# Optimization experiments

Measured on AMD Instinct MI355X. Metric: run time of the kernel, lower is better.

## Reference

```python
import jax, jax.numpy as jnp
import numpy as np

B, N, E, P = 8, 4096, 16384, 64   # batch, num_nodes, num_edges, query poses per scene
D, H, MSG, UPD = 256, 512, 256, 254  # node_dim, MLP hidden, msg_sz, update_sz


def setup_inputs() -> dict:
    key = jax.random.key(0)
    ks = jax.random.split(key, 12)
    s = 0.02  # weight scale
    inp = {
        'nodes_states': jax.random.normal(ks[0], (B, N, D), jnp.float32),
        'attn': jax.random.uniform(ks[1], (B, P, N), jnp.float32),
        'W_e1': (jax.random.normal(ks[2], (2 * D, H), jnp.float32) * s),
        'b_e1': jnp.zeros((H,), jnp.float32),
        'W_e2': (jax.random.normal(ks[3], (H, MSG), jnp.float32) * s),
        'b_e2': jnp.zeros((MSG,), jnp.float32),
        'W_n1': (jax.random.normal(ks[4], (D + MSG, H), jnp.float32) * s),
        'b_n1': jnp.zeros((H,), jnp.float32),
        'W_n2': (jax.random.normal(ks[5], (H, UPD), jnp.float32) * s),
        'b_n2': jnp.zeros((UPD,), jnp.float32),
        'edge_sources': jax.random.randint(ks[6], (E,), 0, N, jnp.int32),
        'edge_sinks': jax.random.randint(ks[7], (E,), 0, N, jnp.int32),
        'msg_steps': 3,
    }
    return inp


def reference(nodes_states, attn, W_e1, b_e1, W_e2, b_e2, W_n1, b_n1, W_n2, b_n2,
              edge_sources, edge_sinks, msg_steps):
    ns = nodes_states  # (B, N, D)
    upd_sz = W_n2.shape[-1]
    for _ in range(int(msg_steps)):
        # gather node states along edges
        src = ns[:, edge_sources]            # (B, E, D)
        snk = ns[:, edge_sinks]              # (B, E, D)
        e_in = jnp.concatenate([src, snk], axis=-1)          # (B, E, 2D)
        h = jax.nn.relu(e_in @ W_e1 + b_e1)
        msgs = h @ W_e2 + b_e2                               # (B, E, MSG)
        # scatter-add messages to sink nodes (== torch index_add on dim 1)
        incoming = jnp.zeros((ns.shape[0], ns.shape[1], msgs.shape[-1]), ns.dtype)
        incoming = incoming.at[:, edge_sinks].add(msgs)      # (B, N, MSG)
        # node update MLP
        n_in = jnp.concatenate([incoming, ns], axis=-1)      # (B, N, D+MSG)
        h2 = jax.nn.relu(n_in @ W_n1 + b_n1)
        upd = h2 @ W_n2 + b_n2                               # (B, N, UPD)
        ns = ns.at[:, :, -upd_sz:].add(upd)
    # graph_out_to_out: attention-weighted extraction (torch.bmm)
    extraction = jnp.einsum('bpn,bnd->bpd', attn, ns)        # (B, P, D)
    # num_copies = 0 -> extraction unchanged; unsqueeze(-1).unsqueeze(-1)
    return extraction[..., None, None]
```

## Files before the change

kernel.cpp:

```cpp
#include <hip/hip_runtime.h>
#include <cstddef>
#include <cstdint>

typedef unsigned short u16;
typedef unsigned int u32;
typedef short bf16x8 __attribute__((ext_vector_type(8)));
typedef float f32x4 __attribute__((ext_vector_type(4)));
typedef u32 u32x4 __attribute__((ext_vector_type(4)));

namespace {
constexpr int B_ = 8, N_ = 4096, E_ = 16384, P_ = 64;
constexpr int D_ = 256, H_ = 512, MSG_ = 256, UPD_ = 254;
constexpr int CHUNK_U16 = 16384;
constexpr int NCHUNK = 24;
constexpr float FXS = 16384.0f;
constexpr float FXI = 1.0f / 16384.0f;
}

__device__ inline u16 f2b(float f) {
  u32 u = __float_as_uint(f);
  u += 0x7FFFu + ((u >> 16) & 1u);
  return (u16)(u >> 16);
}
__device__ inline u32 pk2(float a, float b) {
  return (u32)f2b(a) | ((u32)f2b(b) << 16);
}
__device__ inline f32x4 mfma16(bf16x8 a, bf16x8 b, f32x4 c) {
  return __builtin_amdgcn_mfma_f32_16x16x32_bf16(a, b, c, 0, 0, 0);
}
__device__ inline void gload16(const void* g, void* l) {
  __builtin_amdgcn_global_load_lds(
      (const __attribute__((address_space(1))) unsigned int*)g,
      (__attribute__((address_space(3))) unsigned int*)l, 16, 0, 0);
}
__device__ inline void wait_vm0()   { asm volatile("s_waitcnt vmcnt(0)" ::: "memory"); }
__device__ inline void wait_lgkm0() { asm volatile("s_waitcnt lgkmcnt(0)" ::: "memory"); }
__device__ inline void chunk_boundary() {
  wait_lgkm0();
  wait_vm0();
  __builtin_amdgcn_s_barrier();
  __builtin_amdgcn_sched_barrier(0);
}

__device__ inline int wperm(int s) {
  return (s < 16) ? ((s >> 2) * 8 + (s & 3)) : (((s - 16) >> 2) * 8 + 4 + (s & 3));
}

__global__ void hist_k(const int* __restrict__ esnk, int* __restrict__ cnt) {
  const int e = blockIdx.x * 256 + threadIdx.x;
  atomicAdd(&cnt[esnk[e]], 1);
}
__global__ __launch_bounds__(256)
void scan_k(const int* __restrict__ cnt, int* __restrict__ rowptr,
            int* __restrict__ cursor) {
  __shared__ int part[257];
  const int t = threadIdx.x;
  int c[16]; int s = 0;
#pragma unroll
  for (int i = 0; i < 16; i++) { c[i] = cnt[t * 16 + i]; s += c[i]; }
  part[t + 1] = s;
  __syncthreads();
  if (t == 0) { part[0] = 0; for (int i = 1; i <= 256; i++) part[i] += part[i - 1]; }
  __syncthreads();
  int off = part[t];
#pragma unroll
  for (int i = 0; i < 16; i++) {
    rowptr[t * 16 + i] = off; cursor[t * 16 + i] = off; off += c[i];
  }
}
__global__ void place_k(const int* __restrict__ esnk, int* __restrict__ cursor,
                        int* __restrict__ order) {
  const int e = blockIdx.x * 256 + threadIdx.x;
  const int p = atomicAdd(&cursor[esnk[e]], 1);
  order[p] = e;
}

__global__ void ns_init_k(const float* __restrict__ src, float* __restrict__ ns,
                          u16* __restrict__ dst) {
  const int i = blockIdx.x * 256 + threadIdx.x;
  const float4 v0 = ((const float4*)src)[i * 2];
  const float4 v1 = ((const float4*)src)[i * 2 + 1];
  ((float4*)ns)[i * 2]     = v0;
  ((float4*)ns)[i * 2 + 1] = v1;
  u32x4 pk;
  pk.x = pk2(v0.x, v0.y); pk.y = pk2(v0.z, v0.w);
  pk.z = pk2(v1.x, v1.y); pk.w = pk2(v1.z, v1.w);
  ((u32x4*)dst)[i] = pk;
}

__global__ __launch_bounds__(256, 2)
void edge_mlp(const u16* __restrict__ nsb, u16* __restrict__ msgs,
              const int* __restrict__ esrc, const int* __restrict__ esnk,
              const u16* __restrict__ wpk,
              const float* __restrict__ b1, const float* __restrict__ b2, int g0)
{
  __shared__ alignas(16) u16 Wbuf[2 * CHUNK_U16];

  const int t = threadIdx.x;
  const int w = t >> 6, l = t & 63, r = l & 15, lq = l >> 4;
  const int bl = blockIdx.y, bb = g0 + bl;
  const int e0 = blockIdx.x * 128 + w * 32 + r;
  const int e1 = e0 + 16;

  auto stage1 = [&](int c, int s) {
    const u16* gb = wpk + (size_t)c * CHUNK_U16;
    u16* lb = &Wbuf[(c & 1) * CHUNK_U16];
    const int sidx = s * 256 + t;
    gload16(gb + (size_t)sidx * 8, lb + sidx * 8);
  };
#pragma unroll
  for (int s = 0; s < 8; s++) stage1(0, s);

  const int nrs0 = esrc[e0], nrk0 = esnk[e0];
  const int nrs1 = esrc[e1], nrk1 = esnk[e1];

  bf16x8 af[2][16];
#pragma unroll
  for (int kt = 0; kt < 16; kt++) {
    const int co = (kt < 8 ? kt : kt - 8) * 32 + lq * 8;
    const int n0 = (kt < 8) ? nrs0 : nrk0;
    const int n1 = (kt < 8) ? nrs1 : nrk1;
    af[0][kt] = *(const bf16x8*)(nsb + ((size_t)bb * N_ + n0) * 256 + co);
    af[1][kt] = *(const bf16x8*)(nsb + ((size_t)bb * N_ + n1) * 256 + co);
  }
  chunk_boundary();

  auto mk = [&](f32x4 a0, f32x4 a1, float4 bv0, float4 bv1) -> bf16x8 {
    u32x4 hb;
    hb.x = pk2(fmaxf(a0[0] + bv0.x, 0.f), fmaxf(a0[1] + bv0.y, 0.f));
    hb.y = pk2(fmaxf(a0[2] + bv0.z, 0.f), fmaxf(a0[3] + bv0.w, 0.f));
    hb.z = pk2(fmaxf(a1[0] + bv1.x, 0.f), fmaxf(a1[1] + bv1.y, 0.f));
    hb.w = pk2(fmaxf(a1[2] + bv1.z, 0.f), fmaxf(a1[3] + bv1.w, 0.f));
    return __builtin_bit_cast(bf16x8, hb);
  };

  bf16x8 hB[2][16];

#pragma unroll
  for (int P = 0; P < 16; P++) {
    f32x4 a00 = {}, a01 = {}, a10 = {}, a11 = {};
    const u16* wb = &Wbuf[(P & 1) * CHUNK_U16];
    __builtin_amdgcn_s_setprio(1);
#pragma unroll
    for (int kt = 0; kt < 16; kt++) {
      if (kt < 8) stage1(P + 1, kt);
      const bf16x8 w0 = *(const bf16x8*)&wb[((kt * 2 + 0) * 64 + l) * 8];
      const bf16x8 w1 = *(const bf16x8*)&wb[((kt * 2 + 1) * 64 + l) * 8];
      a00 = mfma16(w0, af[0][kt], a00);
      a01 = mfma16(w1, af[0][kt], a01);
      a10 = mfma16(w0, af[1][kt], a10);
      a11 = mfma16(w1, af[1][kt], a11);
    }
    __builtin_amdgcn_s_setprio(0);
    chunk_boundary();
    const float4 bv0 = *(const float4*)(b1 + P * 32 + lq * 8);
    const float4 bv1 = *(const float4*)(b1 + P * 32 + lq * 8 + 4);
    hB[0][P] = mk(a00, a01, bv0, bv1);
    hB[1][P] = mk(a10, a11, bv0, bv1);
  }

  u16* mrow0 = msgs + ((size_t)bl * E_ + e0) * 256;
  u16* mrow1 = msgs + ((size_t)bl * E_ + e1) * 256;
#pragma unroll
  for (int Hh = 0; Hh < 2; Hh++) {
    f32x4 acc[4][2][2] = {};
#pragma unroll
    for (int cc = 0; cc < 4; cc++) {
      const int C = Hh * 4 + cc, c = 16 + C;
      const u16* wb = &Wbuf[(c & 1) * CHUNK_U16];
      __builtin_amdgcn_s_setprio(1);
#pragma unroll
      for (int kt = 0; kt < 16; kt++) {
        if (kt < 8 && C < 7) stage1(c + 1, kt);
        const bf16x8 w0 = *(const bf16x8*)&wb[((kt * 2 + 0) * 64 + l) * 8];
        const bf16x8 w1 = *(const bf16x8*)&wb[((kt * 2 + 1) * 64 + l) * 8];
        acc[cc][0][0] = mfma16(w0, hB[0][kt], acc[cc][0][0]);
        acc[cc][0][1] = mfma16(w1, hB[0][kt], acc[cc][0][1]);
        acc[cc][1][0] = mfma16(w0, hB[1][kt], acc[cc][1][0]);
        acc[cc][1][1] = mfma16(w1, hB[1][kt], acc[cc][1][1]);
      }
      __builtin_amdgcn_s_setprio(0);
      if (C < 7) chunk_boundary();
    }
#pragma unroll
    for (int cc = 0; cc < 4; cc++) {
      const int C = Hh * 4 + cc;
      const float4 bv0 = *(const float4*)(b2 + C * 32 + lq * 4);
      const float4 bv1 = *(const float4*)(b2 + C * 32 + 16 + lq * 4);
      uint2 q0, q1;
      q0.x = pk2(acc[cc][0][0][0] + bv0.x, acc[cc][0][0][1] + bv0.y);
      q0.y = pk2(acc[cc][0][0][2] + bv0.z, acc[cc][0][0][3] + bv0.w);
      q1.x = pk2(acc[cc][0][1][0] + bv1.x, acc[cc][0][1][1] + bv1.y);
      q1.y = pk2(acc[cc][0][1][2] + bv1.z, acc[cc][0][1][3] + bv1.w);
      *(uint2*)&mrow0[C * 32 + lq * 4]      = q0;
      *(uint2*)&mrow0[C * 32 + 16 + lq * 4] = q1;
      uint2 r0, r1;
      r0.x = pk2(acc[cc][1][0][0] + bv0.x, acc[cc][1][0][1] + bv0.y);
      r0.y = pk2(acc[cc][1][0][2] + bv0.z, acc[cc][1][0][3] + bv0.w);
      r1.x = pk2(acc[cc][1][1][0] + bv1.x, acc[cc][1][1][1] + bv1.y);
      r1.y = pk2(acc[cc][1][1][2] + bv1.z, acc[cc][1][1][3] + bv1.w);
      *(uint2*)&mrow1[C * 32 + lq * 4]      = r0;
      *(uint2*)&mrow1[C * 32 + 16 + lq * 4] = r1;
    }
  }
}

__global__ __launch_bounds__(256)
void gather_k(const u16* __restrict__ msgs, u16* __restrict__ incb,
              const int* __restrict__ order, const int* __restrict__ rowptr,
              const int* __restrict__ cnt, int g0)
{
  const int t = threadIdx.x;
  const int n = blockIdx.x * 4 + (t >> 6);
  const int l = t & 63;
  const int bl = blockIdx.y, bb = g0 + bl;
  const int c0 = l * 4;
  int sA = 0, sB = 0, sC = 0, sD = 0;
  const int beg = rowptr[n], num = cnt[n];
  for (int i = 0; i < num; i++) {
    const int e = order[beg + i];
    const uint2 p = *(const uint2*)(msgs + ((size_t)bl * E_ + e) * 256 + c0);
    sA += __float2int_rn(__uint_as_float(p.x << 16) * FXS);
    sB += __float2int_rn(__uint_as_float(p.x & 0xFFFF0000u) * FXS);
    sC += __float2int_rn(__uint_as_float(p.y << 16) * FXS);
    sD += __float2int_rn(__uint_as_float(p.y & 0xFFFF0000u) * FXS);
  }
  uint2 o;
  o.x = pk2((float)sA * FXI, (float)sB * FXI);
  o.y = pk2((float)sC * FXI, (float)sD * FXI);
  *(uint2*)(incb + ((size_t)bb * N_ + n) * 256 + c0) = o;
}

__global__ __launch_bounds__(128, 1)
void node_mlp(float* __restrict__ ns, u16* __restrict__ nsb,
              const u16* __restrict__ incb, const u16* __restrict__ wpk,
              const float* __restrict__ b1, const float* __restrict__ b2)
{
  __shared__ alignas(16) u16 Wbuf[2 * CHUNK_U16];

  const int t = threadIdx.x;
  const int w = t >> 6, l = t & 63, r = l & 15, lq = l >> 4;
  const int bb = blockIdx.y;
  const int row0 = blockIdx.x * 64 + w * 32 + r;
  const int row1 = row0 + 16;

  auto stage1 = [&](int c, int s) {
    const u16* gb = wpk + (size_t)c * CHUNK_U16;
    u16* lb = &Wbuf[(c & 1) * CHUNK_U16];
    const int sidx = s * 128 + t;
    gload16(gb + (size_t)sidx * 8, lb + sidx * 8);
  };
#pragma unroll
  for (int s = 0; s < 16; s++) stage1(0, s);

  bf16x8 af[2][16];
#pragma unroll
  for (int kt = 0; kt < 16; kt++) {
    if (kt < 8) {
      af[0][kt] = *(const bf16x8*)(incb + ((size_t)bb * N_ + row0) * 256 + kt * 32 + lq * 8);
      af[1][kt] = *(const bf16x8*)(incb + ((size_t)bb * N_ + row1) * 256 + kt * 32 + lq * 8);
    } else {
      const int co = (kt - 8) * 32 + lq * 8;
      af[0][kt] = *(const bf16x8*)(nsb + ((size_t)bb * N_ + row0) * 256 + co);
      af[1][kt] = *(const bf16x8*)(nsb + ((size_t)bb * N_ + row1) * 256 + co);
    }
  }
  chunk_boundary();

  auto mk = [&](f32x4 a0, f32x4 a1, float4 bv0, float4 bv1) -> bf16x8 {
    u32x4 hb;
    hb.x = pk2(fmaxf(a0[0] + bv0.x, 0.f), fmaxf(a0[1] + bv0.y, 0.f));
    hb.y = pk2(fmaxf(a0[2] + bv0.z, 0.f), fmaxf(a0[3] + bv0.w, 0.f));
    hb.z = pk2(fmaxf(a1[0] + bv1.x, 0.f), fmaxf(a1[1] + bv1.y, 0.f));
    hb.w = pk2(fmaxf(a1[2] + bv1.z, 0.f), fmaxf(a1[3] + bv1.w, 0.f));
    return __builtin_bit_cast(bf16x8, hb);
  };

  bf16x8 hB[2][16];

#pragma unroll
  for (int P = 0; P < 16; P++) {
    f32x4 a00 = {}, a01 = {}, a10 = {}, a11 = {};
    const u16* wb = &Wbuf[(P & 1) * CHUNK_U16];
    __builtin_amdgcn_s_setprio(1);
#pragma unroll
    for (int kt = 0; kt < 16; kt++) {
      stage1(P + 1, kt);
      const bf16x8 w0 = *(const bf16x8*)&wb[((kt * 2 + 0) * 64 + l) * 8];
      const bf16x8 w1 = *(const bf16x8*)&wb[((kt * 2 + 1) * 64 + l) * 8];
      a00 = mfma16(w0, af[0][kt], a00);
      a01 = mfma16(w1, af[0][kt], a01);
      a10 = mfma16(w0, af[1][kt], a10);
      a11 = mfma16(w1, af[1][kt], a11);
    }
    __builtin_amdgcn_s_setprio(0);
    chunk_boundary();
    const float4 bv0 = *(const float4*)(b1 + P * 32 + lq * 8);
    const float4 bv1 = *(const float4*)(b1 + P * 32 + lq * 8 + 4);
    hB[0][P] = mk(a00, a01, bv0, bv1);
    hB[1][P] = mk(a10, a11, bv0, bv1);
  }

  float* nsrow0 = ns + ((size_t)bb * N_ + row0) * 256;
  float* nsrow1 = ns + ((size_t)bb * N_ + row1) * 256;
  u16* mbrow0 = nsb + ((size_t)bb * N_ + row0) * 256;
  u16* mbrow1 = nsb + ((size_t)bb * N_ + row1) * 256;
#pragma unroll
  for (int Hh = 0; Hh < 2; Hh++) {
    f32x4 acc[4][2][2] = {};
#pragma unroll
    for (int cc = 0; cc < 4; cc++) {
      const int C = Hh * 4 + cc, c = 16 + C;
      const u16* wb = &Wbuf[(c & 1) * CHUNK_U16];
      __builtin_amdgcn_s_setprio(1);
#pragma unroll
      for (int kt = 0; kt < 16; kt++) {
        if (C < 7) stage1(c + 1, kt);
        const bf16x8 w0 = *(const bf16x8*)&wb[((kt * 2 + 0) * 64 + l) * 8];
        const bf16x8 w1 = *(const bf16x8*)&wb[((kt * 2 + 1) * 64 + l) * 8];
        acc[cc][0][0] = mfma16(w0, hB[0][kt], acc[cc][0][0]);
        acc[cc][0][1] = mfma16(w1, hB[0][kt], acc[cc][0][1]);
        acc[cc][1][0] = mfma16(w0, hB[1][kt], acc[cc][1][0]);
        acc[cc][1][1] = mfma16(w1, hB[1][kt], acc[cc][1][1]);
      }
      __builtin_amdgcn_s_setprio(0);
      if (C < 7) chunk_boundary();
    }
#pragma unroll
    for (int cc = 0; cc < 4; cc++) {
      const int C = Hh * 4 + cc;
      const float4 bv0 = *(const float4*)(b2 + C * 32 + lq * 4);
      const float4 bv1 = *(const float4*)(b2 + C * 32 + 16 + lq * 4);
      const int uA = C * 32 + lq * 4, uB = uA + 16;
#pragma unroll
      for (int g = 0; g < 2; g++) {
        float* nsrow = g ? nsrow1 : nsrow0;
        u16* mrow = g ? mbrow1 : mbrow0;
        const f32x4 a0 = acc[cc][g][0], a1 = acc[cc][g][1];
        float2* pA = (float2*)(nsrow + 2 + uA);
        float2 v0 = pA[0]; v0.x += a0[0] + bv0.x; v0.y += a0[1] + bv0.y; pA[0] = v0;
        float2 v1 = pA[1]; v1.x += a0[2] + bv0.z; v1.y += a0[3] + bv0.w; pA[1] = v1;
        *(u32*)(mrow + 2 + uA)     = pk2(v0.x, v0.y);
        *(u32*)(mrow + 2 + uA + 2) = pk2(v1.x, v1.y);
        float2* pB = (float2*)(nsrow + 2 + uB);
        float2 u0 = pB[0]; u0.x += a1[0] + bv1.x; u0.y += a1[1] + bv1.y; pB[0] = u0;
        *(u32*)(mrow + 2 + uB) = pk2(u0.x, u0.y);
        if (uB + 3 < UPD_) {
          float2 u1 = pB[1]; u1.x += a1[2] + bv1.z; u1.y += a1[3] + bv1.w; pB[1] = u1;
          *(u32*)(mrow + 2 + uB + 2) = pk2(u1.x, u1.y);
        }
      }
    }
  }
}

__global__ void pack_w(const float* __restrict__ W1, const float* __restrict__ W2,
                       int ldw2, int nv2, u16* __restrict__ out)
{
  const int idx = blockIdx.x * 256 + threadIdx.x;
  const int c = idx >> 11, s = idx & 2047;
  const int kt = s >> 7, i01 = (s >> 6) & 1, l = s & 63;
  const int r = l & 15, lq = l >> 4;
  const int kbase = kt * 32 + lq * 8;
  const int colt = i01 * 16 + r;
  u16 v[8];
  if (c < 16) {
    const int col = c * 32 + wperm(colt);
#pragma unroll
    for (int i = 0; i < 8; i++) v[i] = f2b(W1[(size_t)(kbase + i) * 512 + col]);
  } else {
    const int n2 = (c - 16) * 32 + colt;
#pragma unroll
    for (int i = 0; i < 8; i++)
      v[i] = (n2 < nv2) ? f2b(W2[(size_t)(kbase + i) * ldw2 + n2]) : (u16)0;
  }
  u32x4 pk;
  pk.x = (u32)v[0] | ((u32)v[1] << 16);
  pk.y = (u32)v[2] | ((u32)v[3] << 16);
  pk.z = (u32)v[4] | ((u32)v[5] << 16);
  pk.w = (u32)v[6] | ((u32)v[7] << 16);
  *(u32x4*)(out + (size_t)idx * 8) = pk;
}

__global__ __launch_bounds__(256)
void extract_k(const float* __restrict__ attn, const float* __restrict__ nsb,
               float* __restrict__ out)
{
  __shared__ float a_s[16][64];
  const int b = blockIdx.x, pc = blockIdx.y, kc = blockIdx.z;
  const int d = threadIdx.x;
  float acc[16] = {};
  const int nbase0 = kc * 128;

  for (int nb = 0; nb < 128; nb += 64) {
    const int nbase = nbase0 + nb;
    __syncthreads();
#pragma unroll
    for (int lp = 0; lp < 4; lp++) {
      const int idx = lp * 256 + threadIdx.x;
      const int pi = idx >> 6, j = idx & 63;
      a_s[pi][j] = attn[((size_t)b * P_ + pc * 16 + pi) * N_ + nbase + j];
    }
    __syncthreads();
#pragma unroll 8
    for (int j = 0; j < 64; j++) {
      const float v = nsb[((size_t)b * N_ + nbase + j) * D_ + d];
#pragma unroll
      for (int i = 0; i < 16; i++) acc[i] += a_s[i][j] * v;
    }
  }
#pragma unroll
  for (int i = 0; i < 16; i++)
    atomicAdd(&out[((size_t)b * P_ + pc * 16 + i) * D_ + d], acc[i]);
}

extern "C" void kernel_launch(void* const* d_in, const int* in_sizes, int n_in,
                              void* d_out, int out_size, void* d_ws, size_t ws_size,
                              hipStream_t stream)
{
  const float* nodes = (const float*)d_in[0];
  const float* attn  = (const float*)d_in[1];
  const float* W_e1  = (const float*)d_in[2];
  const float* b_e1  = (const float*)d_in[3];
  const float* W_e2  = (const float*)d_in[4];
  const float* b_e2  = (const float*)d_in[5];
  const float* W_n1  = (const float*)d_in[6];
  const float* b_n1  = (const float*)d_in[7];
  const float* W_n2  = (const float*)d_in[8];
  const float* b_n2  = (const float*)d_in[9];
  const int* esrc    = (const int*)d_in[10];
  const int* esnk    = (const int*)d_in[11];

  float* ns   = (float*)d_ws;
  u16* incb   = (u16*)(ns + (size_t)B_ * N_ * D_);
  u16* nsb16  = incb + (size_t)B_ * N_ * MSG_;
  u16* msgs   = nsb16 + (size_t)B_ * N_ * D_;

  const size_t fixed_b = (size_t)B_ * N_ * D_ * 4 + (size_t)B_ * N_ * MSG_ * 2
                       + (size_t)B_ * N_ * D_ * 2
                       + (size_t)2 * NCHUNK * CHUNK_U16 * 2 + (size_t)16 * N_ + 4096;
  int gb = 2;
  if (ws_size >= fixed_b + (size_t)8 * E_ * MSG_ * 2)      gb = 8;
  else if (ws_size >= fixed_b + (size_t)4 * E_ * MSG_ * 2) gb = 4;

  u16* wpkE   = msgs + (size_t)gb * E_ * MSG_;
  u16* wpkN   = wpkE + (size_t)NCHUNK * CHUNK_U16;
  int* cnt    = (int*)(wpkN + (size_t)NCHUNK * CHUNK_U16);
  int* rowptr = cnt + N_;
  int* cursor = rowptr + N_;
  int* order  = cursor + N_;
  float* out  = (float*)d_out;

  ns_init_k<<<dim3(B_ * N_ * D_ / 8 / 256), dim3(256), 0, stream>>>(nodes, ns, nsb16);
  pack_w<<<dim3(192), dim3(256), 0, stream>>>(W_e1, W_e2, MSG_, MSG_, wpkE);
  pack_w<<<dim3(192), dim3(256), 0, stream>>>(W_n1, W_n2, UPD_, UPD_, wpkN);

  hipMemsetAsync(cnt, 0, sizeof(int) * N_, stream);
  hist_k<<<dim3(E_ / 256), dim3(256), 0, stream>>>(esnk, cnt);
  scan_k<<<dim3(1), dim3(256), 0, stream>>>(cnt, rowptr, cursor);
  place_k<<<dim3(E_ / 256), dim3(256), 0, stream>>>(esnk, cursor, order);

  for (int s = 0; s < 3; s++) {
    for (int g0 = 0; g0 < B_; g0 += gb) {
      edge_mlp<<<dim3(E_ / 128, gb), dim3(256), 0, stream>>>(
          nsb16, msgs, esrc, esnk, wpkE, b_e1, b_e2, g0);
      gather_k<<<dim3(N_ / 4, gb), dim3(256), 0, stream>>>(
          msgs, incb, order, rowptr, cnt, g0);
    }
    node_mlp<<<dim3(N_ / 64, B_), dim3(128), 0, stream>>>(
        ns, nsb16, incb, wpkN, b_n1, b_n2);
  }

  hipMemsetAsync(out, 0, sizeof(float) * (size_t)out_size, stream);
  extract_k<<<dim3(B_, P_ / 16, 32), dim3(256), 0, stream>>>(attn, ns, out);
}
```

Baseline: 840.2 us.

## Precompute per-node first-layer projections instead of per-edge first layer GEMM

Splits the edge MLP's first layer algebraically: since concat(src,snk)@W_e1 = src@W_top + snk@W_bot, a new uv_k kernel computes U=ns@W_top and V=ns@W_bot per node (N rows instead of E), and edge_l2 gathers U[src]+V[snk], adds the bias and applies ReLU before the second layer. This halves the first-layer FLOPs (N=4096 versus E=16384 rows, with double output width) at the cost of an extra bf16 intermediate buffer and an extra rounding of U and V to bf16 before summation. Max batch group size drops from 8 to 4 because of the added workspace.

```diff
diff --git a/kernel.cpp b/kernel.cpp
--- a/kernel.cpp
+++ b/kernel.cpp
@@ -12,7 +12,7 @@
 constexpr int B_ = 8, N_ = 4096, E_ = 16384, P_ = 64;
 constexpr int D_ = 256, H_ = 512, MSG_ = 256, UPD_ = 254;
 constexpr int CHUNK_U16 = 16384;
-constexpr int NCHUNK = 24;
+constexpr int UVCHUNK_U16 = 8192;
 constexpr float FXS = 16384.0f;
 constexpr float FXI = 1.0f / 16384.0f;
 }
@@ -25,6 +25,8 @@
 __device__ inline u32 pk2(float a, float b) {
   return (u32)f2b(a) | ((u32)f2b(b) << 16);
 }
+__device__ inline float blo(u32 a) { return __uint_as_float(a << 16); }
+__device__ inline float bhi(u32 a) { return __uint_as_float(a & 0xFFFF0000u); }
 __device__ inline f32x4 mfma16(bf16x8 a, bf16x8 b, f32x4 c) {
   return __builtin_amdgcn_mfma_f32_16x16x32_bf16(a, b, c, 0, 0, 0);
 }
@@ -39,6 +41,11 @@
   wait_lgkm0();
   wait_vm0();
   __builtin_amdgcn_s_barrier();
+  __builtin_amdgcn_sched_barrier(0);
+}
+__device__ inline void wave_boundary() {
+  wait_lgkm0();
+  wait_vm0();
   __builtin_amdgcn_sched_barrier(0);
 }
 
@@ -88,17 +95,86 @@
   ((u32x4*)dst)[i] = pk;
 }
 
+__global__ __launch_bounds__(64)
+void uv_k(const u16* __restrict__ nsb, u16* __restrict__ uvb,
+          const u16* __restrict__ wpkUV, int g0)
+{
+  __shared__ alignas(16) u16 Wbuf[2 * UVCHUNK_U16];
+
+  const int l = threadIdx.x, r = l & 15, lq = l >> 4;
+  const int bl = blockIdx.y, bb = g0 + bl;
+  const int row0 = blockIdx.x * 32 + r, row1 = row0 + 16;
+
+  auto stage1 = [&](int c, int s) {
+    const u16* gb = wpkUV + (size_t)c * UVCHUNK_U16;
+    u16* lb = &Wbuf[(c & 1) * UVCHUNK_U16];
+    const int sidx = s * 64 + l;
+    gload16(gb + (size_t)sidx * 8, lb + sidx * 8);
+  };
+#pragma unroll
+  for (int s = 0; s < 16; s++) stage1(0, s);
+
+  bf16x8 af[2][8];
+#pragma unroll
+  for (int kt = 0; kt < 8; kt++) {
+    af[0][kt] = *(const bf16x8*)(nsb + ((size_t)bb * N_ + row0) * 256 + kt * 32 + lq * 8);
+    af[1][kt] = *(const bf16x8*)(nsb + ((size_t)bb * N_ + row1) * 256 + kt * 32 + lq * 8);
+  }
+  wave_boundary();
+
+  u16* uvrow0 = uvb + ((size_t)bl * N_ + row0) * 1024;
+  u16* uvrow1 = uvb + ((size_t)bl * N_ + row1) * 1024;
+
+#pragma unroll
+  for (int G = 0; G < 8; G++) {
+    f32x4 acc[4][2][2] = {};
+#pragma unroll
+    for (int cc = 0; cc < 4; cc++) {
+      const int c = G * 4 + cc;
+      const u16* wb = &Wbuf[(c & 1) * UVCHUNK_U16];
+      __builtin_amdgcn_s_setprio(1);
+#pragma unroll
+      for (int kt = 0; kt < 8; kt++) {
+        if (c + 1 < 32) { stage1(c + 1, kt * 2); stage1(c + 1, kt * 2 + 1); }
+        const bf16x8 w0 = *(const bf16x8*)&wb[((kt * 2 + 0) * 64 + l) * 8];
+        const bf16x8 w1 = *(const bf16x8*)&wb[((kt * 2 + 1) * 64 + l) * 8];
+        acc[cc][0][0] = mfma16(w0, af[0][kt], acc[cc][0][0]);
+        acc[cc][0][1] = mfma16(w1, af[0][kt], acc[cc][0][1]);
+        acc[cc][1][0] = mfma16(w0, af[1][kt], acc[cc][1][0]);
+        acc[cc][1][1] = mfma16(w1, af[1][kt], acc[cc][1][1]);
+      }
+      __builtin_amdgcn_s_setprio(0);
+      if (c < 31) wave_boundary();
+    }
+#pragma unroll
+    for (int cc = 0; cc < 4; cc++) {
+      const int c = G * 4 + cc;
+#pragma unroll
+      for (int g = 0; g < 2; g++) {
+        u16* mrow = g ? uvrow1 : uvrow0;
+        uint2 q0, q1;
+        q0.x = pk2(acc[cc][g][0][0], acc[cc][g][0][1]);
+        q0.y = pk2(acc[cc][g][0][2], acc[cc][g][0][3]);
+        q1.x = pk2(acc[cc][g][1][0], acc[cc][g][1][1]);
+        q1.y = pk2(acc[cc][g][1][2], acc[cc][g][1][3]);
+        *(uint2*)&mrow[c * 32 + lq * 4]      = q0;
+        *(uint2*)&mrow[c * 32 + 16 + lq * 4] = q1;
+      }
+    }
+  }
+}
+
 __global__ __launch_bounds__(256, 2)
-void edge_mlp(const u16* __restrict__ nsb, u16* __restrict__ msgs,
-              const int* __restrict__ esrc, const int* __restrict__ esnk,
-              const u16* __restrict__ wpk,
-              const float* __restrict__ b1, const float* __restrict__ b2, int g0)
+void edge_l2(const u16* __restrict__ uvb, u16* __restrict__ msgs,
+             const int* __restrict__ esrc, const int* __restrict__ esnk,
+             const u16* __restrict__ wpk,
+             const float* __restrict__ b1, const float* __restrict__ b2, int g0)
 {
   __shared__ alignas(16) u16 Wbuf[2 * CHUNK_U16];
 
   const int t = threadIdx.x;
   const int w = t >> 6, l = t & 63, r = l & 15, lq = l >> 4;
-  const int bl = blockIdx.y, bb = g0 + bl;
+  const int bl = blockIdx.y;
   const int e0 = blockIdx.x * 128 + w * 32 + r;
   const int e1 = e0 + 16;
 
@@ -109,55 +185,39 @@
     gload16(gb + (size_t)sidx * 8, lb + sidx * 8);
   };
 #pragma unroll
-  for (int s = 0; s < 8; s++) stage1(0, s);
+  for (int s = 0; s < 8; s++) stage1(16, s);
 
   const int nrs0 = esrc[e0], nrk0 = esnk[e0];
   const int nrs1 = esrc[e1], nrk1 = esnk[e1];
 
-  bf16x8 af[2][16];
+  const u16* U0 = uvb + ((size_t)bl * N_ + nrs0) * 1024;
+  const u16* V0 = uvb + ((size_t)bl * N_ + nrk0) * 1024 + 512;
+  const u16* U1 = uvb + ((size_t)bl * N_ + nrs1) * 1024;
+  const u16* V1 = uvb + ((size_t)bl * N_ + nrk1) * 1024 + 512;
+
+  bf16x8 hB[2][16];
 #pragma unroll
   for (int kt = 0; kt < 16; kt++) {
-    const int co = (kt < 8 ? kt : kt - 8) * 32 + lq * 8;
-    const int n0 = (kt < 8) ? nrs0 : nrk0;
-    const int n1 = (kt < 8) ? nrs1 : nrk1;
-    af[0][kt] = *(const bf16x8*)(nsb + ((size_t)bb * N_ + n0) * 256 + co);
-    af[1][kt] = *(const bf16x8*)(nsb + ((size_t)bb * N_ + n1) * 256 + co);
+    const int off = kt * 32 + lq * 8;
+    const float4 bA = *(const float4*)(b1 + off);
+    const float4 bB = *(const float4*)(b1 + off + 4);
+    const float bb[8] = {bA.x, bA.y, bA.z, bA.w, bB.x, bB.y, bB.z, bB.w};
+#pragma unroll
+    for (int g = 0; g < 2; g++) {
+      const u32x4 uu = *(const u32x4*)((g ? U1 : U0) + off);
+      const u32x4 vv = *(const u32x4*)((g ? V1 : V0) + off);
+      u32x4 hb;
+#pragma unroll
+      for (int j = 0; j < 4; j++) {
+        const u32 a = uu[j], b = vv[j];
+        const float lo = fmaxf(blo(a) + blo(b) + bb[2 * j], 0.f);
+        const float hi = fmaxf(bhi(a) + bhi(b) + bb[2 * j + 1], 0.f);
+        hb[j] = pk2(lo, hi);
+      }
+      hB[g][kt] = __builtin_bit_cast(bf16x8, hb);
+    }
   }
   chunk_boundary();
-
-  auto mk = [&](f32x4 a0, f32x4 a1, float4 bv0, float4 bv1) -> bf16x8 {
-    u32x4 hb;
-    hb.x = pk2(fmaxf(a0[0] + bv0.x, 0.f), fmaxf(a0[1] + bv0.y, 0.f));
-    hb.y = pk2(fmaxf(a0[2] + bv0.z, 0.f), fmaxf(a0[3] + bv0.w, 0.f));
-    hb.z = pk2(fmaxf(a1[0] + bv1.x, 0.f), fmaxf(a1[1] + bv1.y, 0.f));
-    hb.w = pk2(fmaxf(a1[2] + bv1.z, 0.f), fmaxf(a1[3] + bv1.w, 0.f));
-    return __builtin_bit_cast(bf16x8, hb);
-  };
-
-  bf16x8 hB[2][16];
-
-#pragma unroll
-  for (int P = 0; P < 16; P++) {
-    f32x4 a00 = {}, a01 = {}, a10 = {}, a11 = {};
-    const u16* wb = &Wbuf[(P & 1) * CHUNK_U16];
-    __builtin_amdgcn_s_setprio(1);
-#pragma unroll
-    for (int kt = 0; kt < 16; kt++) {
-      if (kt < 8) stage1(P + 1, kt);
-      const bf16x8 w0 = *(const bf16x8*)&wb[((kt * 2 + 0) * 64 + l) * 8];
-      const bf16x8 w1 = *(const bf16x8*)&wb[((kt * 2 + 1) * 64 + l) * 8];
-      a00 = mfma16(w0, af[0][kt], a00);
-      a01 = mfma16(w1, af[0][kt], a01);
-      a10 = mfma16(w0, af[1][kt], a10);
-      a11 = mfma16(w1, af[1][kt], a11);
-    }
-    __builtin_amdgcn_s_setprio(0);
-    chunk_boundary();
-    const float4 bv0 = *(const float4*)(b1 + P * 32 + lq * 8);
-    const float4 bv1 = *(const float4*)(b1 + P * 32 + lq * 8 + 4);
-    hB[0][P] = mk(a00, a01, bv0, bv1);
-    hB[1][P] = mk(a10, a11, bv0, bv1);
-  }
 
   u16* mrow0 = msgs + ((size_t)bl * E_ + e0) * 256;
   u16* mrow1 = msgs + ((size_t)bl * E_ + e1) * 256;
@@ -382,6 +442,29 @@
   *(u32x4*)(out + (size_t)idx * 8) = pk;
 }
 
+__global__ void pack_uv(const float* __restrict__ W1, u16* __restrict__ out)
+{
+  const int idx = blockIdx.x * 256 + threadIdx.x;
+  const int c = idx >> 10, s = idx & 1023;
+  const int kt = s >> 7, i01 = (s >> 6) & 1, l = s & 63;
+  const int r = l & 15, lq = l >> 4;
+  const int kbase = kt * 32 + lq * 8;
+  const int col = c * 32 + i01 * 16 + r;
+  u16 v[8];
+#pragma unroll
+  for (int i = 0; i < 8; i++) {
+    const int k = kbase + i;
+    v[i] = (col < 512) ? f2b(W1[(size_t)k * 512 + col])
+                       : f2b(W1[(size_t)(256 + k) * 512 + (col - 512)]);
+  }
+  u32x4 pk;
+  pk.x = (u32)v[0] | ((u32)v[1] << 16);
+  pk.y = (u32)v[2] | ((u32)v[3] << 16);
+  pk.z = (u32)v[4] | ((u32)v[5] << 16);
+  pk.w = (u32)v[6] | ((u32)v[7] << 16);
+  *(u32x4*)(out + (size_t)idx * 8) = pk;
+}
+
 __global__ __launch_bounds__(256)
 void extract_k(const float* __restrict__ attn, const float* __restrict__ nsb,
                float* __restrict__ out)
@@ -431,21 +514,22 @@
   const int* esrc    = (const int*)d_in[10];
   const int* esnk    = (const int*)d_in[11];
 
+  const size_t base_b = (size_t)B_ * N_ * D_ * 4 + (size_t)B_ * N_ * MSG_ * 2
+                      + (size_t)B_ * N_ * D_ * 2
+                      + (size_t)2 * 24 * CHUNK_U16 * 2 + (size_t)32 * UVCHUNK_U16 * 2
+                      + (size_t)16 * N_ + 4096;
+  const size_t per_gb = (size_t)E_ * MSG_ * 2 + (size_t)N_ * 1024 * 2;
+  const int gb = (ws_size >= base_b + 4 * per_gb) ? 4 : 2;
+
   float* ns   = (float*)d_ws;
   u16* incb   = (u16*)(ns + (size_t)B_ * N_ * D_);
   u16* nsb16  = incb + (size_t)B_ * N_ * MSG_;
   u16* msgs   = nsb16 + (size_t)B_ * N_ * D_;
-
-  const size_t fixed_b = (size_t)B_ * N_ * D_ * 4 + (size_t)B_ * N_ * MSG_ * 2
-                       + (size_t)B_ * N_ * D_ * 2
-                       + (size_t)2 * NCHUNK * CHUNK_U16 * 2 + (size_t)16 * N_ + 4096;
-  int gb = 2;
-  if (ws_size >= fixed_b + (size_t)8 * E_ * MSG_ * 2)      gb = 8;
-  else if (ws_size >= fixed_b + (size_t)4 * E_ * MSG_ * 2) gb = 4;
-
-  u16* wpkE   = msgs + (size_t)gb * E_ * MSG_;
-  u16* wpkN   = wpkE + (size_t)NCHUNK * CHUNK_U16;
-  int* cnt    = (int*)(wpkN + (size_t)NCHUNK * CHUNK_U16);
+  u16* uvb    = msgs + (size_t)gb * E_ * MSG_;
+  u16* wpkE   = uvb + (size_t)gb * N_ * 1024;
+  u16* wpkN   = wpkE + (size_t)24 * CHUNK_U16;
+  u16* wpkUV  = wpkN + (size_t)24 * CHUNK_U16;
+  int* cnt    = (int*)(wpkUV + (size_t)32 * UVCHUNK_U16);
   int* rowptr = cnt + N_;
   int* cursor = rowptr + N_;
   int* order  = cursor + N_;
@@ -454,6 +538,7 @@
   ns_init_k<<<dim3(B_ * N_ * D_ / 8 / 256), dim3(256), 0, stream>>>(nodes, ns, nsb16);
   pack_w<<<dim3(192), dim3(256), 0, stream>>>(W_e1, W_e2, MSG_, MSG_, wpkE);
   pack_w<<<dim3(192), dim3(256), 0, stream>>>(W_n1, W_n2, UPD_, UPD_, wpkN);
+  pack_uv<<<dim3(128), dim3(256), 0, stream>>>(W_e1, wpkUV);
 
   hipMemsetAsync(cnt, 0, sizeof(int) * N_, stream);
   hist_k<<<dim3(E_ / 256), dim3(256), 0, stream>>>(esnk, cnt);
@@ -462,8 +547,9 @@
 
   for (int s = 0; s < 3; s++) {
     for (int g0 = 0; g0 < B_; g0 += gb) {
-      edge_mlp<<<dim3(E_ / 128, gb), dim3(256), 0, stream>>>(
-          nsb16, msgs, esrc, esnk, wpkE, b_e1, b_e2, g0);
+      uv_k<<<dim3(N_ / 32, gb), dim3(64), 0, stream>>>(nsb16, uvb, wpkUV, g0);
+      edge_l2<<<dim3(E_ / 128, gb), dim3(256), 0, stream>>>(
+          uvb, msgs, esrc, esnk, wpkE, b_e1, b_e2, g0);
       gather_k<<<dim3(N_ / 4, gb), dim3(256), 0, stream>>>(
           msgs, incb, order, rowptr, cnt, g0);
     }
```

Result: no change. 844.1 us (+0.5%).
